# Kernel optimization log

Measured on AMD Instinct MI355X. Metric: run time of the kernel, lower is better.

The kernel has to match this reference:

```python
import jax, jax.numpy as jnp
import numpy as np

U = 359347   # user_num (hardcoded in source)
I = 292589   # item_num (hardcoded in source)
D = 64       # factor_num
NNZ = 4_000_000
B = 32768
LAM = 0.001  # lamada


def setup_inputs() -> dict:
    key = jax.random.key(0)
    ks = jax.random.split(key, 19)
    return {
        "ui_rows": jax.random.randint(ks[0], (NNZ,), 0, U, dtype=jnp.int32),
        "ui_cols": jax.random.randint(ks[1], (NNZ,), 0, I, dtype=jnp.int32),
        "ui_vals": jax.random.uniform(ks[2], (NNZ,), dtype=jnp.float32),
        "iu_vals": jax.random.uniform(ks[3], (NNZ,), dtype=jnp.float32),
        "d_i": jax.random.uniform(ks[4], (U,), dtype=jnp.float32),
        "d_j": jax.random.uniform(ks[5], (I,), dtype=jnp.float32),
        "embed_user": jax.random.normal(ks[6], (U, D), dtype=jnp.float32) * 0.01,
        "embed_item": jax.random.normal(ks[7], (I, D), dtype=jnp.float32) * 0.01,
        "add_w": jax.random.normal(ks[8], (1, 3), dtype=jnp.float32),
        "fw1": jax.random.normal(ks[9], (2 * D, D), dtype=jnp.float32) * (1.0 / np.sqrt(D)),
        "fb1": jax.random.normal(ks[10], (2 * D,), dtype=jnp.float32) * 0.01,
        "fw2": jax.random.normal(ks[11], (D, 2 * D), dtype=jnp.float32) * (1.0 / np.sqrt(2 * D)),
        "fb2": jax.random.normal(ks[12], (D,), dtype=jnp.float32) * 0.01,
        "user_bias": jax.random.normal(ks[13], (U, 1), dtype=jnp.float32) * 0.01,
        "item_bias": jax.random.normal(ks[14], (I, 1), dtype=jnp.float32) * 0.01,
        "avg_rating": jax.random.uniform(ks[15], (1,), dtype=jnp.float32) * 5.0,
        "user0": jax.random.randint(ks[16], (B,), 0, U, dtype=jnp.int32),
        "item_i0": jax.random.randint(ks[17], (B,), 0, I, dtype=jnp.int32),
        "ratings": jax.random.uniform(ks[18], (B,), dtype=jnp.float32) * 5.0,
    }


def _spmm(rows, cols, vals, x, num_rows):
    # sparse [num_rows, *] COO @ dense x : gather rows of x by col index,
    # scale by edge value, scatter-add into destination rows.
    return jax.ops.segment_sum(vals[:, None] * x[cols], rows, num_segments=num_rows)


def _leaky(x):
    return jnp.where(x > 0, x, 0.1 * x)


def _user_filter(x, fw1, fb1, fw2, fb2):
    h = _leaky(x @ fw1.T + fb1)
    return _leaky(h @ fw2.T + fb2)


def reference(ui_rows, ui_cols, ui_vals, iu_vals, d_i, d_j,
              embed_user, embed_item, add_w, fw1, fb1, fw2, fb2,
              user_bias, item_bias, avg_rating, user0, item_i0, ratings):
    ue, ie = embed_user, embed_item
    # layer 1: SpMM + degree-scaled residual + ReLU
    g1_u = jax.nn.relu(_spmm(ui_rows, ui_cols, ui_vals, ie, U) + ue * d_i[:, None])
    g1_i = jax.nn.relu(_spmm(ui_cols, ui_rows, iu_vals, ue, I) + ie * d_j[:, None])
    # layer 2
    g2_u = jax.nn.relu(_spmm(ui_rows, ui_cols, ui_vals, g1_i, U) + g1_u * d_i[:, None])
    g2_i = jax.nn.relu(_spmm(ui_cols, ui_rows, iu_vals, g1_u, I) + g1_i * d_j[:, None])
    # learned combination of the 3 layers: Linear(3,1) over the stacked axis
    w = add_w[0]  # [3]
    gcn_u = w[0] * ue + w[1] * g1_u + w[2] * g2_u   # [U, D]
    gcn_i = w[0] * ie + w[1] * g1_i + w[2] * g2_i   # [I, D]
    # batch lookup + shared filter MLP
    user = _user_filter(gcn_u[user0], fw1, fb1, fw2, fb2)      # [B, D]
    item = _user_filter(gcn_i[item_i0], fw1, fb1, fw2, fb2)    # [B, D]
    pred = (user * item).sum(-1) + user_bias[user0, 0] + item_bias[item_i0, 0] + avg_rating
    l2 = LAM * jnp.mean(gcn_u ** 2) + LAM * jnp.mean(gcn_i ** 2)
    loss2 = jnp.mean((pred - ratings) ** 2)
    return loss2 + l2
```

## Files before the change

kernel.cpp:

```cpp
#include <hip/hip_runtime.h>

#define U_NUM 359347
#define I_NUM 292589
#define DDIM  64
#define NNZ_N 4000000
#define BATCH 32768
#define LAM_F 0.001f
#define ACC_SLOTS 2048

#define EPB   4096
#define NBLK  ((NNZ_N + EPB - 1) / EPB)
#define NB_U  ((U_NUM + 1023) >> 10)
#define NB_I  ((I_NUM + 1023) >> 10)

__device__ __forceinline__ float leaky(float x) { return x > 0.f ? x : 0.1f * x; }

__device__ __forceinline__ unsigned short f2bf(float f) {
    unsigned b = __float_as_uint(f);
    b = (b + 0x7FFF + ((b >> 16) & 1)) >> 16;
    return (unsigned short)b;
}
__device__ __forceinline__ float bf2f(unsigned short u) {
    return __uint_as_float((unsigned)u << 16);
}
__device__ __forceinline__ float bflo(unsigned u) { return __uint_as_float(u << 16); }
__device__ __forceinline__ float bfhi(unsigned u) { return __uint_as_float(u & 0xffff0000u); }

__device__ __forceinline__ unsigned char f2fp8(float v) {
    v = fminf(fmaxf(v * 64.f, -440.f), 440.f);
    unsigned b = __float_as_uint(v * 0x1p-120f);
    unsigned sign = (b >> 24) & 0x80u;
    unsigned mag = b & 0x7fffffffu;
    mag += 0x7ffffu + ((mag >> 20) & 1u);
    return (unsigned char)(sign | ((mag >> 20) & 0x7fu));
}
#if __has_builtin(__builtin_amdgcn_cvt_f32_fp8)
#define FP8DEC(b) __builtin_amdgcn_cvt_f32_fp8((int)(b), 0)
#else
#define FP8DEC(b) (__uint_as_float(((unsigned)((b) & 0x80u) << 24) | \
                                   ((unsigned)((b) & 0x7fu) << 20)) * 0x1p120f)
#endif
#define INV64 0.015625f

__global__ __launch_bounds__(256) void f2f8_k(
    const float4* __restrict__ inU, uchar4* __restrict__ o8U,
    const float4* __restrict__ inI, uchar4* __restrict__ o8I,
    size_t nU4, size_t total4)
{
    size_t stride = (size_t)gridDim.x * 256;
    for (size_t i = (size_t)blockIdx.x * 256 + threadIdx.x; i < total4; i += stride) {
        const float4* in; uchar4* o8; size_t j;
        if (i < nU4) { in = inU; o8 = o8U; j = i; }
        else         { in = inI; o8 = o8I; j = i - nU4; }
        float4 v = in[j];
        uchar4 p;
        p.x = f2fp8(v.x); p.y = f2fp8(v.y); p.z = f2fp8(v.z); p.w = f2fp8(v.w);
        o8[j] = p;
    }
}

__global__ __launch_bounds__(256) void hist2_k(
    const int* __restrict__ rows, const int* __restrict__ cols,
    int* __restrict__ gh_u, int* __restrict__ gh_i)
{
    __shared__ int h[512];
    int sideB = blockIdx.x >= NBLK;
    int blk = sideB ? blockIdx.x - NBLK : blockIdx.x;
    const int* keys = sideB ? cols : rows;
    int nb = sideB ? NB_I : NB_U;
    int* gh = sideB ? gh_i : gh_u;
    for (int i = threadIdx.x; i < nb; i += 256) h[i] = 0;
    __syncthreads();
    int base = blk * EPB;
    int end = min(base + EPB, NNZ_N);
    for (int e = base + threadIdx.x; e < end; e += 256)
        atomicAdd(&h[keys[e] >> 10], 1);
    __syncthreads();
    for (int i = threadIdx.x; i < nb; i += 256)
        gh[i * NBLK + blk] = h[i];
}

__global__ __launch_bounds__(256) void scan1m_k(
    int* __restrict__ aU, int nUe, int* __restrict__ bsU, int nb1U,
    int* __restrict__ aI, int nIe, int* __restrict__ bsI)
{
    __shared__ int s[256];
    int sideB = (int)blockIdx.x >= nb1U;
    int blk = sideB ? blockIdx.x - nb1U : blockIdx.x;
    int* a = sideB ? aI : aU;
    int n = sideB ? nIe : nUe;
    int* bsum = sideB ? bsI : bsU;
    int t = threadIdx.x;
    int base = blk * 1024 + t * 4;
    int v[4];
#pragma unroll
    for (int j = 0; j < 4; ++j) v[j] = (base + j < n) ? a[base + j] : 0;
    s[t] = v[0] + v[1] + v[2] + v[3];
    __syncthreads();
    for (int off = 1; off < 256; off <<= 1) {
        int x = (t >= off) ? s[t - off] : 0;
        __syncthreads();
        s[t] += x;
        __syncthreads();
    }
    if (t == 255) bsum[blk] = s[255];
    int run = (t > 0) ? s[t - 1] : 0;
#pragma unroll
    for (int j = 0; j < 4; ++j) {
        if (base + j < n) a[base + j] = run;
        run += v[j];
    }
}

__global__ __launch_bounds__(512) void scan2m_k(
    int* __restrict__ bsU, int nbU, int* __restrict__ bsI, int nbI)
{
    __shared__ int s[512];
    int* bsum = blockIdx.x ? bsI : bsU;
    int nb = blockIdx.x ? nbI : nbU;
    int t = threadIdx.x;
    int v = (t < nb) ? bsum[t] : 0;
    s[t] = v;
    __syncthreads();
    for (int off = 1; off < 512; off <<= 1) {
        int x = (t >= off) ? s[t - off] : 0;
        __syncthreads();
        s[t] += x;
        __syncthreads();
    }
    if (t < nb) bsum[t] = s[t] - v;
}

__global__ __launch_bounds__(256) void scan3m_k(
    int* __restrict__ aU, int nUe, const int* __restrict__ bsU, int nb1U,
    int* __restrict__ aI, int nIe, const int* __restrict__ bsI)
{
    int sideB = (int)blockIdx.x >= nb1U;
    int blk = sideB ? blockIdx.x - nb1U : blockIdx.x;
    int* a = sideB ? aI : aU;
    int n = sideB ? nIe : nUe;
    int add = (sideB ? bsI : bsU)[blk];
    int base = blk * 1024 + threadIdx.x * 4;
#pragma unroll
    for (int j = 0; j < 4; ++j)
        if (base + j < n) a[base + j] += add;
}

__global__ __launch_bounds__(256) void scat2_k(
    const int* __restrict__ rows, const int* __restrict__ cols,
    const float* __restrict__ uv, const float* __restrict__ iv,
    const int* __restrict__ gh_u, const int* __restrict__ gh_i,
    unsigned* __restrict__ tc_u, unsigned short* __restrict__ tv_u,
    unsigned* __restrict__ tc_i, unsigned short* __restrict__ tv_i)
{
    __shared__ int cur[512];
    int sideB = blockIdx.x >= NBLK;
    int blk = sideB ? blockIdx.x - NBLK : blockIdx.x;
    const int* keys = sideB ? cols : rows;
    const int* other = sideB ? rows : cols;
    const float* vals = sideB ? iv : uv;
    const int* gh = sideB ? gh_i : gh_u;
    int nb = sideB ? NB_I : NB_U;
    unsigned* tc = sideB ? tc_i : tc_u;
    unsigned short* tv = sideB ? tv_i : tv_u;
    for (int i = threadIdx.x; i < nb; i += 256) cur[i] = gh[i * NBLK + blk];
    __syncthreads();
    int base = blk * EPB;
    int end = min(base + EPB, NNZ_N);
    for (int e = base + threadIdx.x; e < end; e += 256) {
        int k = keys[e];
        int pos = atomicAdd(&cur[k >> 10], 1);
        tc[pos] = ((unsigned)other[e] << 10) | (unsigned)(k & 1023);
        tv[pos] = f2bf(vals[e] * INV64);
    }
}

__global__ __launch_bounds__(256) void l2sort2_k(
    const unsigned* __restrict__ tc_u, const unsigned short* __restrict__ tv_u,
    const unsigned* __restrict__ tc_i, const unsigned short* __restrict__ tv_i,
    const int* __restrict__ gh_u, const int* __restrict__ gh_i,
    int* __restrict__ ptr_u, int* __restrict__ ptr_i,
    int* __restrict__ ecol_u, unsigned short* __restrict__ eval_u,
    int* __restrict__ ecol_i, unsigned short* __restrict__ eval_i)
{
    __shared__ int hist[1024];
    __shared__ int ssc[256];
    int sideB = blockIdx.x >= NB_U;
    int b = sideB ? blockIdx.x - NB_U : blockIdx.x;
    const unsigned* tc = sideB ? tc_i : tc_u;
    const unsigned short* tv = sideB ? tv_i : tv_u;
    const int* gh = sideB ? gh_i : gh_u;
    int nb = sideB ? NB_I : NB_U;
    int nrows = sideB ? I_NUM : U_NUM;
    int* ptr = sideB ? ptr_i : ptr_u;
    int* ecol = sideB ? ecol_i : ecol_u;
    unsigned short* eval = sideB ? eval_i : eval_u;
    int t = threadIdx.x;
    int bucket_base = gh[b * NBLK];
    int bucket_end  = (b == nb - 1) ? NNZ_N : gh[(b + 1) * NBLK];
    for (int i = t; i < 1024; i += 256) hist[i] = 0;
    __syncthreads();
    for (int e = bucket_base + t; e < bucket_end; e += 256)
        atomicAdd(&hist[tc[e] & 1023u], 1);
    __syncthreads();
    int v0 = hist[t * 4], v1 = hist[t * 4 + 1], v2 = hist[t * 4 + 2], v3 = hist[t * 4 + 3];
    ssc[t] = v0 + v1 + v2 + v3;
    __syncthreads();
    for (int off = 1; off < 256; off <<= 1) {
        int x = (t >= off) ? ssc[t - off] : 0;
        __syncthreads();
        ssc[t] += x;
        __syncthreads();
    }
    int run = (t > 0) ? ssc[t - 1] : 0;
    int g0 = run, g1 = run + v0, g2 = g1 + v1, g3 = g2 + v2;
    hist[t * 4] = g0; hist[t * 4 + 1] = g1; hist[t * 4 + 2] = g2; hist[t * 4 + 3] = g3;
    int rbase = b << 10;
    if (rbase + t * 4 < nrows)     ptr[rbase + t * 4]     = bucket_base + g0;
    if (rbase + t * 4 + 1 < nrows) ptr[rbase + t * 4 + 1] = bucket_base + g1;
    if (rbase + t * 4 + 2 < nrows) ptr[rbase + t * 4 + 2] = bucket_base + g2;
    if (rbase + t * 4 + 3 < nrows) ptr[rbase + t * 4 + 3] = bucket_base + g3;
    if (b == nb - 1 && t == 0) ptr[nrows] = NNZ_N;
    __syncthreads();
    for (int e = bucket_base + t; e < bucket_end; e += 256) {
        unsigned q = tc[e];
        int pos = bucket_base + atomicAdd(&hist[q & 1023u], 1);
        ecol[pos] = (int)(q >> 10);
        eval[pos] = tv[e];
    }
}

template <int MODE>
__global__ __launch_bounds__(256) void spmm_dual_k(
    int gA,
    const int* __restrict__ ptrA, const int* __restrict__ ecolA, const unsigned short* __restrict__ evalA,
    const unsigned char* __restrict__ x8A, const unsigned char* __restrict__ base8A,
    const float* __restrict__ degA, int nA,
    unsigned char* __restrict__ out8A, unsigned short* __restrict__ outbA,
    const unsigned char* __restrict__ emb8A, float* __restrict__ accA,
    const int* __restrict__ ptrB, const int* __restrict__ ecolB, const unsigned short* __restrict__ evalB,
    const unsigned char* __restrict__ x8B, const unsigned char* __restrict__ base8B,
    const float* __restrict__ degB, int nB,
    unsigned char* __restrict__ out8B, unsigned short* __restrict__ outbB,
    const unsigned char* __restrict__ emb8B, float* __restrict__ accB,
    const float* __restrict__ add_w)
{
    int wv = threadIdx.x >> 6, lane = threadIdx.x & 63;
    int bid = blockIdx.x;
    int sideB = bid >= gA;
    int lb = sideB ? bid - gA : bid;
    const int* ptr = sideB ? ptrB : ptrA;
    const int* ecol = sideB ? ecolB : ecolA;
    const unsigned short* eval = sideB ? evalB : evalA;
    const unsigned char* x8 = sideB ? x8B : x8A;
    const unsigned char* base8 = sideB ? base8B : base8A;
    const float* deg = sideB ? degB : degA;
    int nrows = sideB ? nB : nA;
    __shared__ float ssum[4];
    int r = lb * 4 + wv;
    if (r < nrows) {
        int s0 = __builtin_amdgcn_readfirstlane(ptr[r]);
        int e0 = __builtin_amdgcn_readfirstlane(ptr[r + 1]);
        float a0 = 0.f, a1 = 0.f, a2 = 0.f, a3 = 0.f;
        int k = s0;
        for (; k + 8 <= e0; k += 8) {
            int c0 = ecol[k],     c1 = ecol[k + 1], c2 = ecol[k + 2], c3 = ecol[k + 3];
            int c4 = ecol[k + 4], c5 = ecol[k + 5], c6 = ecol[k + 6], c7 = ecol[k + 7];
            unsigned char b0 = x8[(size_t)c0 * DDIM + lane];
            unsigned char b1 = x8[(size_t)c1 * DDIM + lane];
            unsigned char b2 = x8[(size_t)c2 * DDIM + lane];
            unsigned char b3 = x8[(size_t)c3 * DDIM + lane];
            unsigned char b4 = x8[(size_t)c4 * DDIM + lane];
            unsigned char b5 = x8[(size_t)c5 * DDIM + lane];
            unsigned char b6 = x8[(size_t)c6 * DDIM + lane];
            unsigned char b7 = x8[(size_t)c7 * DDIM + lane];
            a0 = fmaf(bf2f(eval[k]),     FP8DEC(b0), a0);
            a1 = fmaf(bf2f(eval[k + 1]), FP8DEC(b1), a1);
            a2 = fmaf(bf2f(eval[k + 2]), FP8DEC(b2), a2);
            a3 = fmaf(bf2f(eval[k + 3]), FP8DEC(b3), a3);
            a0 = fmaf(bf2f(eval[k + 4]), FP8DEC(b4), a0);
            a1 = fmaf(bf2f(eval[k + 5]), FP8DEC(b5), a1);
            a2 = fmaf(bf2f(eval[k + 6]), FP8DEC(b6), a2);
            a3 = fmaf(bf2f(eval[k + 7]), FP8DEC(b7), a3);
        }
        for (; k + 4 <= e0; k += 4) {
            int c0 = ecol[k], c1 = ecol[k + 1], c2 = ecol[k + 2], c3 = ecol[k + 3];
            unsigned char b0 = x8[(size_t)c0 * DDIM + lane];
            unsigned char b1 = x8[(size_t)c1 * DDIM + lane];
            unsigned char b2 = x8[(size_t)c2 * DDIM + lane];
            unsigned char b3 = x8[(size_t)c3 * DDIM + lane];
            a0 = fmaf(bf2f(eval[k]),     FP8DEC(b0), a0);
            a1 = fmaf(bf2f(eval[k + 1]), FP8DEC(b1), a1);
            a2 = fmaf(bf2f(eval[k + 2]), FP8DEC(b2), a2);
            a3 = fmaf(bf2f(eval[k + 3]), FP8DEC(b3), a3);
        }
        for (; k < e0; ++k)
            a0 = fmaf(bf2f(eval[k]), FP8DEC(x8[(size_t)ecol[k] * DDIM + lane]), a0);
        float acc = (a0 + a1) + (a2 + a3);
        float bb64 = FP8DEC(base8[(size_t)r * DDIM + lane]);
        float o = fmaxf(fmaf(bb64, deg[r] * INV64, acc), 0.f);
        if (MODE == 0) {
            (sideB ? out8B : out8A)[(size_t)r * DDIM + lane] = f2fp8(o);
        } else {
            const unsigned char* emb8 = sideB ? emb8B : emb8A;
            float e64 = FP8DEC(emb8[(size_t)r * DDIM + lane]);
            float g = fmaf(add_w[0] * INV64, e64,
                      fmaf(add_w[1] * INV64, bb64, add_w[2] * o));
            (sideB ? outbB : outbA)[(size_t)r * DDIM + lane] = f2bf(g);
            float sq = g * g;
            for (int off = 32; off; off >>= 1) sq += __shfl_down(sq, off);
            if (lane == 0) ssum[wv] = sq;
        }
    } else if (MODE == 1) {
        if (lane == 0) ssum[wv] = 0.f;
    }
    if (MODE == 1) {
        __syncthreads();
        if (threadIdx.x == 0)
            atomicAdd(&(sideB ? accB : accA)[lb & (ACC_SLOTS - 1)],
                      ssum[0] + ssum[1] + ssum[2] + ssum[3]);
    }
}

__global__ __launch_bounds__(256) void mlp_k(
    const int* __restrict__ user0, const int* __restrict__ item0,
    const unsigned short* __restrict__ gcnU, const unsigned short* __restrict__ gcnI,
    const float* __restrict__ fw1, const float* __restrict__ fb1,
    const float* __restrict__ fw2, const float* __restrict__ fb2,
    unsigned short* __restrict__ ou, unsigned short* __restrict__ oi)
{
    __shared__ unsigned short xs[64][72];
    __shared__ unsigned short w1s[128][68];
    __shared__ unsigned short w2s[64][140];
    __shared__ unsigned short hs[128][72];
    __shared__ float b1s[128];
    __shared__ float b2s[64];

    int t = threadIdx.x;
    int side = blockIdx.x >> 9;
    int tile = blockIdx.x & 511;
    const int* sel = side ? item0 : user0;
    const unsigned short* gcn = side ? gcnI : gcnU;
    unsigned short* outp = side ? oi : ou;

    {
        int r = t >> 2, c = t & 3;
        int idx = sel[tile * 64 + r];
        const ushort4* src = (const ushort4*)(gcn + (size_t)idx * 64 + c * 16);
        ushort4 v0 = src[0], v1 = src[1], v2 = src[2], v3 = src[3];
        int k0 = c * 16;
        xs[k0 +  0][r] = v0.x; xs[k0 +  1][r] = v0.y; xs[k0 +  2][r] = v0.z; xs[k0 +  3][r] = v0.w;
        xs[k0 +  4][r] = v1.x; xs[k0 +  5][r] = v1.y; xs[k0 +  6][r] = v1.z; xs[k0 +  7][r] = v1.w;
        xs[k0 +  8][r] = v2.x; xs[k0 +  9][r] = v2.y; xs[k0 + 10][r] = v2.z; xs[k0 + 11][r] = v2.w;
        xs[k0 + 12][r] = v3.x; xs[k0 + 13][r] = v3.y; xs[k0 + 14][r] = v3.z; xs[k0 + 15][r] = v3.w;
    }
#pragma unroll
    for (int i = 0; i < 8; ++i) {
        int flat = i * 1024 + t * 4;
        float4 w = *(const float4*)(fw1 + flat);
        int o = flat >> 6, k = flat & 63;
        *(unsigned*)&w1s[o][k]     = (unsigned)f2bf(w.x) | ((unsigned)f2bf(w.y) << 16);
        *(unsigned*)&w1s[o][k + 2] = (unsigned)f2bf(w.z) | ((unsigned)f2bf(w.w) << 16);
        float4 u = *(const float4*)(fw2 + flat);
        int o2 = flat >> 7, k2 = flat & 127;
        *(unsigned*)&w2s[o2][k2]     = (unsigned)f2bf(u.x) | ((unsigned)f2bf(u.y) << 16);
        *(unsigned*)&w2s[o2][k2 + 2] = (unsigned)f2bf(u.z) | ((unsigned)f2bf(u.w) << 16);
    }
    if (t < 128) b1s[t] = fb1[t];
    if (t < 64)  b2s[t] = fb2[t];
    __syncthreads();

    int sg = t & 15, og = t >> 4;

    float acc[4][8];
#pragma unroll
    for (int i = 0; i < 4; ++i)
#pragma unroll
        for (int j = 0; j < 8; ++j) acc[i][j] = 0.f;

    for (int kc = 0; kc < 64; kc += 4) {
        uint2 xp0 = *(const uint2*)&xs[kc    ][sg * 4];
        uint2 xp1 = *(const uint2*)&xs[kc + 1][sg * 4];
        uint2 xp2 = *(const uint2*)&xs[kc + 2][sg * 4];
        uint2 xp3 = *(const uint2*)&xs[kc + 3][sg * 4];
        float x0[4] = { bflo(xp0.x), bfhi(xp0.x), bflo(xp0.y), bfhi(xp0.y) };
        float x1[4] = { bflo(xp1.x), bfhi(xp1.x), bflo(xp1.y), bfhi(xp1.y) };
        float x2[4] = { bflo(xp2.x), bfhi(xp2.x), bflo(xp2.y), bfhi(xp2.y) };
        float x3[4] = { bflo(xp3.x), bfhi(xp3.x), bflo(xp3.y), bfhi(xp3.y) };
#pragma unroll
        for (int j = 0; j < 8; ++j) {
            uint2 wp = *(const uint2*)&w1s[og * 8 + j][kc];
            float w0 = bflo(wp.x), w1v = bfhi(wp.x), w2v = bflo(wp.y), w3v = bfhi(wp.y);
#pragma unroll
            for (int i = 0; i < 4; ++i) {
                acc[i][j] = fmaf(x0[i], w0,  acc[i][j]);
                acc[i][j] = fmaf(x1[i], w1v, acc[i][j]);
                acc[i][j] = fmaf(x2[i], w2v, acc[i][j]);
                acc[i][j] = fmaf(x3[i], w3v, acc[i][j]);
            }
        }
    }
#pragma unroll
    for (int j = 0; j < 8; ++j) {
        int o = og * 8 + j;
        float b = b1s[o];
        float h0 = leaky(acc[0][j] + b), h1 = leaky(acc[1][j] + b);
        float h2 = leaky(acc[2][j] + b), h3 = leaky(acc[3][j] + b);
        *(unsigned*)&hs[o][sg * 4]     = (unsigned)f2bf(h0) | ((unsigned)f2bf(h1) << 16);
        *(unsigned*)&hs[o][sg * 4 + 2] = (unsigned)f2bf(h2) | ((unsigned)f2bf(h3) << 16);
    }
    __syncthreads();

    float acc2[4][4];
#pragma unroll
    for (int i = 0; i < 4; ++i)
#pragma unroll
        for (int j = 0; j < 4; ++j) acc2[i][j] = 0.f;

    for (int kc = 0; kc < 128; kc += 4) {
        uint2 hp0 = *(const uint2*)&hs[kc    ][sg * 4];
        uint2 hp1 = *(const uint2*)&hs[kc + 1][sg * 4];
        uint2 hp2 = *(const uint2*)&hs[kc + 2][sg * 4];
        uint2 hp3 = *(const uint2*)&hs[kc + 3][sg * 4];
        float h0[4] = { bflo(hp0.x), bfhi(hp0.x), bflo(hp0.y), bfhi(hp0.y) };
        float h1[4] = { bflo(hp1.x), bfhi(hp1.x), bflo(hp1.y), bfhi(hp1.y) };
        float h2[4] = { bflo(hp2.x), bfhi(hp2.x), bflo(hp2.y), bfhi(hp2.y) };
        float h3[4] = { bflo(hp3.x), bfhi(hp3.x), bflo(hp3.y), bfhi(hp3.y) };
#pragma unroll
        for (int j = 0; j < 4; ++j) {
            uint2 wp = *(const uint2*)&w2s[og * 4 + j][kc];
            float w0 = bflo(wp.x), w1v = bfhi(wp.x), w2v = bflo(wp.y), w3v = bfhi(wp.y);
#pragma unroll
            for (int i = 0; i < 4; ++i) {
                acc2[i][j] = fmaf(h0[i], w0,  acc2[i][j]);
                acc2[i][j] = fmaf(h1[i], w1v, acc2[i][j]);
                acc2[i][j] = fmaf(h2[i], w2v, acc2[i][j]);
                acc2[i][j] = fmaf(h3[i], w3v, acc2[i][j]);
            }
        }
    }
#pragma unroll
    for (int i = 0; i < 4; ++i) {
        float o0 = leaky(acc2[i][0] + b2s[og * 4 + 0]);
        float o1 = leaky(acc2[i][1] + b2s[og * 4 + 1]);
        float o2 = leaky(acc2[i][2] + b2s[og * 4 + 2]);
        float o3 = leaky(acc2[i][3] + b2s[og * 4 + 3]);
        uint2 pp;
        pp.x = (unsigned)f2bf(o0) | ((unsigned)f2bf(o1) << 16);
        pp.y = (unsigned)f2bf(o2) | ((unsigned)f2bf(o3) << 16);
        *(uint2*)(outp + ((size_t)(tile * 64 + sg * 4 + i) * 64 + og * 4)) = pp;
    }
}

__global__ __launch_bounds__(256) void dot_sse_k(
    const unsigned short* __restrict__ ou, const unsigned short* __restrict__ oi,
    const int* __restrict__ user0, const int* __restrict__ item0,
    const float* __restrict__ ub, const float* __restrict__ ib,
    const float* __restrict__ avg, const float* __restrict__ ratings,
    float* __restrict__ sse)
{
    int g = blockIdx.x * 256 + threadIdx.x;
    int b = g >> 2, q = g & 3;
    const uint4* pu = (const uint4*)(ou + (size_t)b * 64 + q * 16);
    const uint4* pi = (const uint4*)(oi + (size_t)b * 64 + q * 16);
    uint4 a0 = pu[0], a1 = pu[1];
    uint4 c0 = pi[0], c1 = pi[1];
    float s = 0.f;
#define DOTP(ua, uc) { s = fmaf(bflo(ua), bflo(uc), s); s = fmaf(bfhi(ua), bfhi(uc), s); }
    DOTP(a0.x, c0.x) DOTP(a0.y, c0.y) DOTP(a0.z, c0.z) DOTP(a0.w, c0.w)
    DOTP(a1.x, c1.x) DOTP(a1.y, c1.y) DOTP(a1.z, c1.z) DOTP(a1.w, c1.w)
#undef DOTP
    s += __shfl_xor(s, 1);
    s += __shfl_xor(s, 2);
    float contrib = 0.f;
    if (q == 0) {
        float pred = s + ub[user0[b]] + ib[item0[b]] + avg[0];
        float d = pred - ratings[b];
        contrib = d * d;
    }
    for (int off = 32; off; off >>= 1) contrib += __shfl_down(contrib, off);
    __shared__ float wsum[4];
    int lane = threadIdx.x & 63, wv = threadIdx.x >> 6;
    if (lane == 0) wsum[wv] = contrib;
    __syncthreads();
    if (threadIdx.x == 0)
        atomicAdd(sse, wsum[0] + wsum[1] + wsum[2] + wsum[3]);
}

__global__ __launch_bounds__(256) void finalize2_k(
    const float* __restrict__ accU, const float* __restrict__ accI,
    const float* __restrict__ sse, float* __restrict__ out)
{
    int t = threadIdx.x;
    float su = 0.f, si = 0.f;
    for (int i = t; i < ACC_SLOTS; i += 256) { su += accU[i]; si += accI[i]; }
    for (int off = 32; off; off >>= 1) {
        su += __shfl_down(su, off);
        si += __shfl_down(si, off);
    }
    __shared__ float s[8];
    int wv = t >> 6, lane = t & 63;
    if (lane == 0) { s[wv] = su; s[wv + 4] = si; }
    __syncthreads();
    if (t == 0) {
        float SU = s[0] + s[1] + s[2] + s[3];
        float SI = s[4] + s[5] + s[6] + s[7];
        out[0] = sse[0] / (float)BATCH
               + LAM_F * (SU / (float)((double)U_NUM * 64.0))
               + LAM_F * (SI / (float)((double)I_NUM * 64.0));
    }
}


extern "C" void kernel_launch(void* const* d_in, const int* in_sizes, int n_in,
                              void* d_out, int out_size, void* d_ws, size_t ws_size,
                              hipStream_t stream)
{
    const int*   ui_rows = (const int*)d_in[0];
    const int*   ui_cols = (const int*)d_in[1];
    const float* ui_vals = (const float*)d_in[2];
    const float* iu_vals = (const float*)d_in[3];
    const float* d_i     = (const float*)d_in[4];
    const float* d_j     = (const float*)d_in[5];
    const float* eu      = (const float*)d_in[6];
    const float* ei      = (const float*)d_in[7];
    const float* add_w   = (const float*)d_in[8];
    const float* fw1     = (const float*)d_in[9];
    const float* fb1     = (const float*)d_in[10];
    const float* fw2     = (const float*)d_in[11];
    const float* fb2     = (const float*)d_in[12];
    const float* ub      = (const float*)d_in[13];
    const float* ib      = (const float*)d_in[14];
    const float* avg     = (const float*)d_in[15];
    const int*   user0   = (const int*)d_in[16];
    const int*   item0   = (const int*)d_in[17];
    const float* ratings = (const float*)d_in[18];

    const size_t U64 = (size_t)U_NUM * DDIM;
    const size_t I64 = (size_t)I_NUM * DDIM;

    int*            ecol_u = (int*)d_ws;
    unsigned short* eval_u = (unsigned short*)(ecol_u + NNZ_N);
    int*            ecol_i = (int*)(eval_u + NNZ_N);
    unsigned short* eval_i = (unsigned short*)(ecol_i + NNZ_N);
    unsigned short* ou_bf  = (unsigned short*)ecol_u;
    unsigned short* oi_bf  = ou_bf + (size_t)BATCH * 64;
    unsigned*       tc_u   = (unsigned*)(eval_i + NNZ_N);
    unsigned short* tv_u   = (unsigned short*)(tc_u + NNZ_N);
    unsigned*       tc_i   = (unsigned*)(tv_u + NNZ_N);
    unsigned short* tv_i   = (unsigned short*)(tc_i + NNZ_N);
    unsigned char*  g1u_f8 = (unsigned char*)tc_u;
    unsigned char*  g1i_f8 = g1u_f8 + ((U64 + 15) & ~15ull);
    int*  gh_u  = (int*)(tv_i + NNZ_N);
    int*  gh_i  = gh_u + (size_t)NB_U * NBLK;
    int*  bsumU = gh_i + (size_t)NB_I * NBLK;
    int*  bsumI = bsumU + 512;
    int*  ptr_u = bsumI + 512;
    int*  ptr_i = ptr_u + (U_NUM + 1);
    float* accU = (float*)(ptr_i + (I_NUM + 1));
    float* accI = accU + ACC_SLOTS;
    float* sse  = accI + ACC_SLOTS;
    unsigned char*  eu_f8  = (unsigned char*)(sse + 4);
    unsigned char*  ei_f8  = eu_f8 + ((U64 + 15) & ~15ull);
    unsigned short* gcnU_bf = (unsigned short*)(ei_f8 + ((I64 + 15) & ~15ull));
    unsigned short* gcnI_bf = gcnU_bf + U64;
    (void)ws_size;

    dim3 blk(256);
    int gu = (U_NUM + 3) / 4, gi = (I_NUM + 3) / 4;
    int nUe = NB_U * NBLK, nIe = NB_I * NBLK;
    int nb1U = (nUe + 1023) / 1024, nb1I = (nIe + 1023) / 1024;

    size_t meta_bytes = ((char*)(sse + 4)) - (char*)gh_u;
    hipMemsetAsync(gh_u, 0, meta_bytes, stream);

    f2f8_k<<<2048, blk, 0, stream>>>((const float4*)eu, (uchar4*)eu_f8,
                                     (const float4*)ei, (uchar4*)ei_f8,
                                     U64 / 4, (U64 + I64) / 4);

    hist2_k<<<2 * NBLK, blk, 0, stream>>>(ui_rows, ui_cols, gh_u, gh_i);
    scan1m_k<<<nb1U + nb1I, blk, 0, stream>>>(gh_u, nUe, bsumU, nb1U, gh_i, nIe, bsumI);
    scan2m_k<<<2, 512, 0, stream>>>(bsumU, nb1U, bsumI, nb1I);
    scan3m_k<<<nb1U + nb1I, blk, 0, stream>>>(gh_u, nUe, bsumU, nb1U, gh_i, nIe, bsumI);

    scat2_k<<<2 * NBLK, blk, 0, stream>>>(ui_rows, ui_cols, ui_vals, iu_vals,
                                          gh_u, gh_i, tc_u, tv_u, tc_i, tv_i);
    l2sort2_k<<<NB_U + NB_I, blk, 0, stream>>>(tc_u, tv_u, tc_i, tv_i, gh_u, gh_i,
                                               ptr_u, ptr_i, ecol_u, eval_u, ecol_i, eval_i);

    spmm_dual_k<0><<<gu + gi, blk, 0, stream>>>(gu,
        ptr_u, ecol_u, eval_u, ei_f8, eu_f8, d_i, U_NUM, g1u_f8, nullptr, nullptr, nullptr,
        ptr_i, ecol_i, eval_i, eu_f8, ei_f8, d_j, I_NUM, g1i_f8, nullptr, nullptr, nullptr,
        nullptr);
    spmm_dual_k<1><<<gi + gu, blk, 0, stream>>>(gi,
        ptr_i, ecol_i, eval_i, g1u_f8, g1i_f8, d_j, I_NUM, nullptr, gcnI_bf, ei_f8, accI,
        ptr_u, ecol_u, eval_u, g1i_f8, g1u_f8, d_i, U_NUM, nullptr, gcnU_bf, eu_f8, accU,
        add_w);

    mlp_k<<<1024, blk, 0, stream>>>(user0, item0, gcnU_bf, gcnI_bf,
                                    fw1, fb1, fw2, fb2, ou_bf, oi_bf);
    dot_sse_k<<<BATCH * 4 / 256, blk, 0, stream>>>(ou_bf, oi_bf, user0, item0,
                                                   ub, ib, avg, ratings, sse);
    finalize2_k<<<1, blk, 0, stream>>>(accU, accI, sse, (float*)d_out);
}
```

Before: 1.157 ms.

## Process four edges per wavefront step with 16 lanes per row and uchar4 gathers

Reworks the CSR SpMM inner loop so each wavefront splits into four 16-lane groups, each handling one edge and loading four FP8 features as a uchar4, instead of all 64 lanes reading single bytes from one edge. Partial sums are combined across groups with xor shuffles, and only group 0 writes the packed output; the squared-norm reduction is rescaled by 0.25 to undo the fourfold replication. The aim is fewer, wider gather instructions and more edges in flight per wavefront. The cost is extra shuffle reductions, redundant epilogue arithmetic in three of the four groups, and a masked tail path.

After: 1.170 ms. About the same (+1.1%).

```diff
diff --git a/kernel.cpp b/kernel.cpp
--- a/kernel.cpp
+++ b/kernel.cpp
@@ -246,6 +246,7 @@
     const float* __restrict__ add_w)
 {
     int wv = threadIdx.x >> 6, lane = threadIdx.x & 63;
+    int g = lane >> 4, sl = lane & 15;
     int bid = blockIdx.x;
     int sideB = bid >= gA;
     int lb = sideB ? bid - gA : bid;
@@ -262,54 +263,78 @@
         int s0 = __builtin_amdgcn_readfirstlane(ptr[r]);
         int e0 = __builtin_amdgcn_readfirstlane(ptr[r + 1]);
         float a0 = 0.f, a1 = 0.f, a2 = 0.f, a3 = 0.f;
+        float b0 = 0.f, b1 = 0.f, b2 = 0.f, b3 = 0.f;
         int k = s0;
         for (; k + 8 <= e0; k += 8) {
-            int c0 = ecol[k],     c1 = ecol[k + 1], c2 = ecol[k + 2], c3 = ecol[k + 3];
-            int c4 = ecol[k + 4], c5 = ecol[k + 5], c6 = ecol[k + 6], c7 = ecol[k + 7];
-            unsigned char b0 = x8[(size_t)c0 * DDIM + lane];
-            unsigned char b1 = x8[(size_t)c1 * DDIM + lane];
-            unsigned char b2 = x8[(size_t)c2 * DDIM + lane];
-            unsigned char b3 = x8[(size_t)c3 * DDIM + lane];
-            unsigned char b4 = x8[(size_t)c4 * DDIM + lane];
-            unsigned char b5 = x8[(size_t)c5 * DDIM + lane];
-            unsigned char b6 = x8[(size_t)c6 * DDIM + lane];
-            unsigned char b7 = x8[(size_t)c7 * DDIM + lane];
-            a0 = fmaf(bf2f(eval[k]),     FP8DEC(b0), a0);
-            a1 = fmaf(bf2f(eval[k + 1]), FP8DEC(b1), a1);
-            a2 = fmaf(bf2f(eval[k + 2]), FP8DEC(b2), a2);
-            a3 = fmaf(bf2f(eval[k + 3]), FP8DEC(b3), a3);
-            a0 = fmaf(bf2f(eval[k + 4]), FP8DEC(b4), a0);
-            a1 = fmaf(bf2f(eval[k + 5]), FP8DEC(b5), a1);
-            a2 = fmaf(bf2f(eval[k + 6]), FP8DEC(b6), a2);
-            a3 = fmaf(bf2f(eval[k + 7]), FP8DEC(b7), a3);
+            int   cA = ecol[k + g];
+            float vA = bf2f(eval[k + g]);
+            int   cB = ecol[k + 4 + g];
+            float vB = bf2f(eval[k + 4 + g]);
+            uchar4 xA = *(const uchar4*)(x8 + (size_t)cA * DDIM + sl * 4);
+            uchar4 xB = *(const uchar4*)(x8 + (size_t)cB * DDIM + sl * 4);
+            a0 = fmaf(vA, FP8DEC(xA.x), a0);
+            a1 = fmaf(vA, FP8DEC(xA.y), a1);
+            a2 = fmaf(vA, FP8DEC(xA.z), a2);
+            a3 = fmaf(vA, FP8DEC(xA.w), a3);
+            b0 = fmaf(vB, FP8DEC(xB.x), b0);
+            b1 = fmaf(vB, FP8DEC(xB.y), b1);
+            b2 = fmaf(vB, FP8DEC(xB.z), b2);
+            b3 = fmaf(vB, FP8DEC(xB.w), b3);
         }
         for (; k + 4 <= e0; k += 4) {
-            int c0 = ecol[k], c1 = ecol[k + 1], c2 = ecol[k + 2], c3 = ecol[k + 3];
-            unsigned char b0 = x8[(size_t)c0 * DDIM + lane];
-            unsigned char b1 = x8[(size_t)c1 * DDIM + lane];
-            unsigned char b2 = x8[(size_t)c2 * DDIM + lane];
-            unsigned char b3 = x8[(size_t)c3 * DDIM + lane];
-            a0 = fmaf(bf2f(eval[k]),     FP8DEC(b0), a0);
-            a1 = fmaf(bf2f(eval[k + 1]), FP8DEC(b1), a1);
-            a2 = fmaf(bf2f(eval[k + 2]), FP8DEC(b2), a2);
-            a3 = fmaf(bf2f(eval[k + 3]), FP8DEC(b3), a3);
+            int   c = ecol[k + g];
+            float v = bf2f(eval[k + g]);
+            uchar4 x = *(const uchar4*)(x8 + (size_t)c * DDIM + sl * 4);
+            a0 = fmaf(v, FP8DEC(x.x), a0);
+            a1 = fmaf(v, FP8DEC(x.y), a1);
+            a2 = fmaf(v, FP8DEC(x.z), a2);
+            a3 = fmaf(v, FP8DEC(x.w), a3);
         }
-        for (; k < e0; ++k)
-            a0 = fmaf(bf2f(eval[k]), FP8DEC(x8[(size_t)ecol[k] * DDIM + lane]), a0);
-        float acc = (a0 + a1) + (a2 + a3);
-        float bb64 = FP8DEC(base8[(size_t)r * DDIM + lane]);
-        float o = fmaxf(fmaf(bb64, deg[r] * INV64, acc), 0.f);
+        if (k < e0) {
+            int idx = k + g;
+            bool on = idx < e0;
+            int   c = ecol[on ? idx : s0];
+            float v = on ? bf2f(eval[idx]) : 0.f;
+            uchar4 x = *(const uchar4*)(x8 + (size_t)c * DDIM + sl * 4);
+            a0 = fmaf(v, FP8DEC(x.x), a0);
+            a1 = fmaf(v, FP8DEC(x.y), a1);
+            a2 = fmaf(v, FP8DEC(x.z), a2);
+            a3 = fmaf(v, FP8DEC(x.w), a3);
+        }
+        a0 += b0; a1 += b1; a2 += b2; a3 += b3;
+        a0 += __shfl_xor(a0, 16); a0 += __shfl_xor(a0, 32);
+        a1 += __shfl_xor(a1, 16); a1 += __shfl_xor(a1, 32);
+        a2 += __shfl_xor(a2, 16); a2 += __shfl_xor(a2, 32);
+        a3 += __shfl_xor(a3, 16); a3 += __shfl_xor(a3, 32);
+
+        uchar4 bb = *(const uchar4*)(base8 + (size_t)r * DDIM + sl * 4);
+        float dg = deg[r] * INV64;
+        float o0 = fmaxf(fmaf(FP8DEC(bb.x), dg, a0), 0.f);
+        float o1 = fmaxf(fmaf(FP8DEC(bb.y), dg, a1), 0.f);
+        float o2 = fmaxf(fmaf(FP8DEC(bb.z), dg, a2), 0.f);
+        float o3 = fmaxf(fmaf(FP8DEC(bb.w), dg, a3), 0.f);
         if (MODE == 0) {
-            (sideB ? out8B : out8A)[(size_t)r * DDIM + lane] = f2fp8(o);
+            if (g == 0) {
+                uchar4 p;
+                p.x = f2fp8(o0); p.y = f2fp8(o1); p.z = f2fp8(o2); p.w = f2fp8(o3);
+                *(uchar4*)((sideB ? out8B : out8A) + (size_t)r * DDIM + sl * 4) = p;
+            }
         } else {
             const unsigned char* emb8 = sideB ? emb8B : emb8A;
-            float e64 = FP8DEC(emb8[(size_t)r * DDIM + lane]);
-            float g = fmaf(add_w[0] * INV64, e64,
-                      fmaf(add_w[1] * INV64, bb64, add_w[2] * o));
-            (sideB ? outbB : outbA)[(size_t)r * DDIM + lane] = f2bf(g);
-            float sq = g * g;
+            uchar4 eb = *(const uchar4*)(emb8 + (size_t)r * DDIM + sl * 4);
+            float w0s = add_w[0] * INV64, w1s = add_w[1] * INV64, w2v = add_w[2];
+            float q0 = fmaf(w0s, FP8DEC(eb.x), fmaf(w1s, FP8DEC(bb.x), w2v * o0));
+            float q1 = fmaf(w0s, FP8DEC(eb.y), fmaf(w1s, FP8DEC(bb.y), w2v * o1));
+            float q2 = fmaf(w0s, FP8DEC(eb.z), fmaf(w1s, FP8DEC(bb.z), w2v * o2));
+            float q3 = fmaf(w0s, FP8DEC(eb.w), fmaf(w1s, FP8DEC(bb.w), w2v * o3));
+            if (g == 0) {
+                ushort4 p;
+                p.x = f2bf(q0); p.y = f2bf(q1); p.z = f2bf(q2); p.w = f2bf(q3);
+                *(ushort4*)((sideB ? outbB : outbA) + (size_t)r * DDIM + sl * 4) = p;
+            }
+            float sq = q0 * q0 + q1 * q1 + q2 * q2 + q3 * q3;
             for (int off = 32; off; off >>= 1) sq += __shfl_down(sq, off);
-            if (lane == 0) ssum[wv] = sq;
+            if (lane == 0) ssum[wv] = sq * 0.25f;
         }
     } else if (MODE == 1) {
         if (lane == 0) ssum[wv] = 0.f;
```
